# Kernel optimization log

Measured on AMD Instinct MI355X. Metric: run time of the kernel, lower is better.

## Reference

```python
import jax, jax.numpy as jnp
import numpy as np
from jax import lax

NUM_CLASSES = 10
NUM_ITERS = 3


def conv2d(x, w, b, stride):
    # x: [B,C,H,W], w: [O,I,kh,kw]
    y = lax.conv_general_dilated(x, w, (stride, stride), 'VALID',
                                 dimension_numbers=('NCHW', 'OIHW', 'NCHW'))
    return y + b[None, :, None, None]


def squash(t, axis=-1):
    sn = jnp.sum(t * t, axis=axis, keepdims=True)
    return (sn / (1.0 + sn)) * t / jnp.sqrt(sn)


def routing(x, W, num_iters=NUM_ITERS):
    # x: [B,R,Ci], W: [C,R,Ci,Co] -> outputs [B,C,Co]
    # priors[c,b,r,o] = sum_i x[b,r,i] * W[c,r,i,o]
    priors = jnp.einsum('bri,crio->cbro', x, W)  # [C,B,R,Co]
    C, B, R, Co = priors.shape
    # torch logits are [C,B,R,1,Co] but identical along Co (zeros init,
    # delta broadcast), so a [C,B,R,1] logit is mathematically identical.
    logits = jnp.zeros((C, B, R, 1), priors.dtype)
    outputs = None
    for i in range(num_iters):
        probs = jax.nn.softmax(logits, axis=2)            # over route nodes
        s = jnp.sum(probs * priors, axis=2, keepdims=True)  # [C,B,1,Co]
        outputs = squash(s, axis=-1)
        if i != num_iters - 1:
            logits = logits + jnp.sum(priors * outputs, axis=-1, keepdims=True)
    return jnp.transpose(outputs[:, :, 0, :], (1, 0, 2))  # [B,C,Co]


def setup_inputs() -> dict:
    key = jax.random.key(0)
    ks = jax.random.split(key, 16)
    B = 32
    s = 0.05
    inp = {
        'x': jax.random.normal(ks[0], (B, 1, 61, 61), jnp.float32),
        'conv0_w': jax.random.normal(ks[1], (256, 1, 9, 9), jnp.float32) * s,
        'conv0_b': jnp.zeros((256,), jnp.float32),
        'conv1_w': jax.random.normal(ks[2], (256, 256, 9, 9), jnp.float32) * s,
        'conv1_b': jnp.zeros((256,), jnp.float32),
        # 8 primary-capsule convs stacked: [8*32, 256, 9, 9]
        'prim_w': jax.random.normal(ks[3], (8 * 32, 256, 9, 9), jnp.float32) * s,
        'prim_b': jnp.zeros((8 * 32,), jnp.float32),
        'W1': jax.random.normal(ks[4], (64, 32 * 6 * 6, 8, 16), jnp.float32) * s,
        'W2': jax.random.normal(ks[5], (NUM_CLASSES, 64, 16, 16), jnp.float32) * s,
        'dec_w1': jax.random.normal(ks[6], (16 * NUM_CLASSES, 1024), jnp.float32) * s,
        'dec_b1': jnp.zeros((1024,), jnp.float32),
        'dec_w2': jax.random.normal(ks[7], (1024, 2048), jnp.float32) * s,
        'dec_b2': jnp.zeros((2048,), jnp.float32),
        'dec_w3': jax.random.normal(ks[8], (2048, 4096), jnp.float32) * s,
        'dec_b3': jnp.zeros((4096,), jnp.float32),
    }
    return inp


def reference(x, conv0_w, conv0_b, conv1_w, conv1_b, prim_w, prim_b,
              W1, W2, dec_w1, dec_b1, dec_w2, dec_b2, dec_w3, dec_b3):
    B = x.shape[0]
    h = jax.nn.relu(conv2d(x, conv0_w, conv0_b, 2))       # [B,256,27,27]
    h = jax.nn.relu(conv2d(h, conv1_w, conv1_b, 1))       # [B,256,19,19]
    # primary capsules: 8 convs of 32 channels each, k9 s2 -> [B,256,6,6]
    p = conv2d(h, prim_w, prim_b, 2)
    # torch: each capsule conv -> view(B, 32*6*6, 1), cat on last -> [B,1152,8]
    p = p.reshape(B, 8, 32 * 6 * 6)                        # [B,8,1152]
    p = jnp.transpose(p, (0, 2, 1))                        # [B,1152,8]
    p = squash(p, axis=-1)
    u = routing(p, W1)                                     # [B,64,16]
    v = routing(u, W2)                                     # [B,10,16]
    classes = jnp.sqrt(jnp.sum(v * v, axis=-1))            # [B,10]
    classes = jax.nn.softmax(classes, axis=-1)
    y = jax.nn.one_hot(jnp.argmax(classes, axis=1), NUM_CLASSES,
                       dtype=v.dtype)                       # [B,10]
    y = lax.stop_gradient(y)
    z = (v * y[:, :, None]).reshape(B, -1)                 # [B,160]
    d = jax.nn.relu(z @ dec_w1 + dec_b1)
    d = jax.nn.relu(d @ dec_w2 + dec_b2)
    reconstructions = jax.nn.sigmoid(d @ dec_w3 + dec_b3)  # [B,4096]
    return classes, reconstructions
```

## Files before the change

### kernel.cpp

```cpp
#include <hip/hip_runtime.h>
#include <hip/hip_bf16.h>
#include <math.h>


#define NB 32

typedef _Float16 f16;
typedef f16 f16x2 __attribute__((ext_vector_type(2)));
typedef f16 f16x4 __attribute__((ext_vector_type(4)));
typedef f16 f16x8 __attribute__((ext_vector_type(8)));
typedef float f32x4 __attribute__((ext_vector_type(4)));

__device__ __forceinline__ int swz(int row, int q) {
  return row * 64 + ((q * 16) ^ (((row >> 1) & 3) << 4));
}

__global__ __launch_bounds__(256) void wprep_kernel(
    const float* __restrict__ w1, const float* __restrict__ w2,
    f16* __restrict__ wo1, f16* __restrict__ wo2) {
  __shared__ f16 tile[256][82];
  int bi = blockIdx.x;
  const float* src;
  f16* dst;
  if (bi < 256) {
    src = w1 + (size_t)bi * 20736;
    dst = wo1 + bi * 256;
  } else {
    src = w2 + (size_t)(bi - 256) * 20736;
    dst = wo2 + (bi - 256) * 256;
  }
  int t = threadIdx.x;
  for (int j = t; j < 20736; j += 256) {
    int r = j / 81, c = j - r * 81;
    tile[r][c] = (f16)src[j];
  }
  __syncthreads();
  f16* d = dst + t;
  for (int tap = 0; tap < 81; ++tap)
    d[(size_t)tap * 65536] = tile[t][tap];
}

__global__ __launch_bounds__(256) void conv0_kernel(
    const float* __restrict__ x, const float* __restrict__ w,
    const float* __restrict__ bias, f16* __restrict__ outf) {
  int b = blockIdx.x, ocg = blockIdx.y, z = blockIdx.z;
  __shared__ float img[61 * 61];
  __shared__ __align__(16) float wl[81][32];
  int t = threadIdx.x;
  for (int i = t; i < 61 * 61; i += 256) img[i] = x[b * 3721 + i];
  for (int i = t; i < 81 * 32; i += 256) {
    int k = i >> 5, oc = i & 31;
    wl[k][oc] = w[(ocg * 32 + oc) * 81 + k];
  }
  __syncthreads();
  int ocs = (t & 7) * 4;
  int pg  = t >> 3;
  int oc0 = ocg * 32 + ocs;
  float b0 = bias[oc0 + 0], b1 = bias[oc0 + 1], b2 = bias[oc0 + 2],
        b3 = bias[oc0 + 3];
  for (int p = pg + z * 32; p < 729; p += 64) {
    int oh = p / 27, ow = p - oh * 27;
    float a0 = 0.f, a1 = 0.f, a2 = 0.f, a3 = 0.f;
    const float* ib = &img[oh * 2 * 61 + ow * 2];
#pragma unroll
    for (int kh = 0; kh < 9; ++kh) {
#pragma unroll
      for (int kw = 0; kw < 9; ++kw) {
        float v = ib[kh * 61 + kw];
        const float4 wv =
            *reinterpret_cast<const float4*>(&wl[kh * 9 + kw][ocs]);
        a0 += v * wv.x; a1 += v * wv.y; a2 += v * wv.z; a3 += v * wv.w;
      }
    }
    int po = oh * 28 + ow;
    f16x4 hv;
    hv[0] = (f16)fmaxf(a0 + b0, 0.f);
    hv[1] = (f16)fmaxf(a1 + b1, 0.f);
    hv[2] = (f16)fmaxf(a2 + b2, 0.f);
    hv[3] = (f16)fmaxf(a3 + b3, 0.f);
    *(f16x4*)&outf[((size_t)b * 756 + po) * 256 + oc0] = hv;
  }
}

__global__ __launch_bounds__(256, 3) void conv1_mfma(
    const f16* __restrict__ xin,
    const f16* __restrict__ wA,
    f16* __restrict__ part) {
  int b = blockIdx.x, ocg = blockIdx.y;
  int ksp = blockIdx.z >> 1, ph = blockIdx.z & 1;
  __shared__ __align__(16) f16 blds[504 * 32];
  __shared__ __align__(16) f16 alds[2][64 * 32];
  int t = threadIdx.x;
  int w = t >> 6, lane = t & 63, kg = lane >> 4, ln = lane & 15;
  int aoc = t >> 2, aq = t & 3;
  int row0 = ph * 252;
  int prow[3];
#pragma unroll
  for (int nf = 0; nf < 3; ++nf) {
    int n = ph * 192 + w * 48 + nf * 16 + ln;
    int oh = n / 20, ow = n - oh * 20;
    if (oh > 18) oh = 18;
    if (ow > 18) ow = 18;
    prow[nf] = oh * 28 + ow - row0;
  }
  f32x4 acc[4][3];
#pragma unroll
  for (int m = 0; m < 4; ++m)
#pragma unroll
    for (int nf = 0; nf < 3; ++nf) acc[m][nf] = (f32x4){0.f, 0.f, 0.f, 0.f};

  const f16* xb = xin + (size_t)b * 756 * 256 + ksp * 64;
  const f16* ab = wA + (size_t)(ocg * 64 + aoc) * 256 + ksp * 64 + aq * 8;
  for (int icc = 0; icc < 2; ++icc) {
    __syncthreads();
    for (int i = t; i < 2016; i += 256) {
      int p = i >> 2, q = i & 3;
      f16x8 v =
          *(const f16x8*)(xb + (size_t)(row0 + p) * 256 + icc * 32 + q * 8);
      *(f16x8*)((char*)blds + swz(p, q)) = v;
    }
    {
      f16x8 v = *(const f16x8*)(ab + icc * 32);
      *(f16x8*)((char*)alds[0] + swz(aoc, aq)) = v;
    }
    __syncthreads();
    for (int tap = 0; tap < 81; ++tap) {
      int cur = tap & 1;
      if (tap < 80) {
        f16x8 v = *(const f16x8*)(ab + (size_t)(tap + 1) * 65536 + icc * 32);
        *(f16x8*)((char*)alds[cur ^ 1] + swz(aoc, aq)) = v;
      }
      int kh = tap / 9, kw = tap - kh * 9;
      int shift = kh * 28 + kw;
      f16x8 af[4];
#pragma unroll
      for (int m = 0; m < 4; ++m)
        af[m] = *(const f16x8*)((const char*)alds[cur] + swz(m * 16 + ln, kg));
      f16x8 bf[3];
#pragma unroll
      for (int nf = 0; nf < 3; ++nf)
        bf[nf] =
            *(const f16x8*)((const char*)blds + swz(prow[nf] + shift, kg));
#pragma unroll
      for (int m = 0; m < 4; ++m)
#pragma unroll
        for (int nf = 0; nf < 3; ++nf)
          acc[m][nf] = __builtin_amdgcn_mfma_f32_16x16x32_f16(
              af[m], bf[nf], acc[m][nf], 0, 0, 0);
      __syncthreads();
    }
  }
  f16* pout = part + ((size_t)ksp * 32 + b) * 384 * 256 + ocg * 64;
#pragma unroll
  for (int m = 0; m < 4; ++m)
#pragma unroll
    for (int nf = 0; nf < 3; ++nf) {
      int n = ph * 192 + w * 48 + nf * 16 + ln;
      int oc = m * 16 + kg * 4;
      f16x4 v;
#pragma unroll
      for (int j = 0; j < 4; ++j) v[j] = (f16)acc[m][nf][j];
      *(f16x4*)(pout + (size_t)n * 256 + oc) = v;
    }
}

__global__ void comb1_kernel(const f16* __restrict__ part,
                             const float* __restrict__ bias,
                             f16* __restrict__ h1f) {
  int idx = blockIdx.x * 256 + threadIdx.x;
  if (idx >= 32 * 380 * 32) return;
  int ocq = idx & 31, rem = idx >> 5;
  int p = rem % 380, b = rem / 380;
  float a[8];
#pragma unroll
  for (int j = 0; j < 8; ++j) a[j] = bias[ocq * 8 + j];
#pragma unroll
  for (int k = 0; k < 4; ++k) {
    f16x8 v = *(const f16x8*)&part[(((size_t)k * 32 + b) * 384 + p) * 256 +
                                   ocq * 8];
#pragma unroll
    for (int j = 0; j < 8; ++j) a[j] += (float)v[j];
  }
  f16x8 o;
#pragma unroll
  for (int j = 0; j < 8; ++j) o[j] = (f16)fmaxf(a[j], 0.f);
  *(f16x8*)&h1f[((size_t)b * 380 + p) * 256 + ocq * 8] = o;
}

__global__ __launch_bounds__(256, 3) void prim_mfma(
    const f16* __restrict__ xin,
    const f16* __restrict__ wB,
    float* __restrict__ part2) {
  int b = blockIdx.x, ocg = blockIdx.y, ksp = blockIdx.z;
  __shared__ __align__(16) f16 blds[384 * 32];
  __shared__ __align__(16) f16 alds[2][128 * 32];
  int t = threadIdx.x;
  int w = t >> 6, lane = t & 63, kg = lane >> 4, ln = lane & 15;
  int rbase[3];
#pragma unroll
  for (int nf = 0; nf < 3; ++nf) {
    int rem = nf * 16 + ln;
    int oh6 = rem >> 3, ow6 = rem & 7;
    rbase[nf] = oh6 * 40 + ow6 * 2;
  }
  f32x4 acc[2][3];
#pragma unroll
  for (int m = 0; m < 2; ++m)
#pragma unroll
    for (int nf = 0; nf < 3; ++nf) acc[m][nf] = (f32x4){0.f, 0.f, 0.f, 0.f};

  for (int i = t; i < 1536; i += 256) {
    int pos = i >> 2, q = i & 3;
    int p = pos < 380 ? pos : pos - 20;
    f16x8 v = *(const f16x8*)(xin + ((size_t)b * 380 + p) * 256 + ksp * 32 +
                              q * 8);
    *(f16x8*)((char*)blds + swz(pos, q)) = v;
  }
  const f16* ab = wB + (size_t)(ocg * 128) * 256 + ksp * 32;
  for (int i = t; i < 512; i += 256) {
    int oc = i >> 2, q = i & 3;
    f16x8 v = *(const f16x8*)(ab + (size_t)oc * 256 + q * 8);
    *(f16x8*)((char*)alds[0] + swz(oc, q)) = v;
  }
  __syncthreads();
  for (int tap = 0; tap < 81; ++tap) {
    int cur = tap & 1;
    if (tap < 80) {
      for (int i = t; i < 512; i += 256) {
        int oc = i >> 2, q = i & 3;
        f16x8 v = *(const f16x8*)(ab + (size_t)(tap + 1) * 65536 +
                                  (size_t)oc * 256 + q * 8);
        *(f16x8*)((char*)alds[cur ^ 1] + swz(oc, q)) = v;
      }
    }
    int kh = tap / 9, kw = tap - kh * 9;
    int shift = kh * 20 + kw;
    f16x8 af[2];
#pragma unroll
    for (int m = 0; m < 2; ++m)
      af[m] = *(const f16x8*)((const char*)alds[cur] +
                              swz((w * 2 + m) * 16 + ln, kg));
    f16x8 bf[3];
#pragma unroll
    for (int nf = 0; nf < 3; ++nf)
      bf[nf] = *(const f16x8*)((const char*)blds + swz(rbase[nf] + shift, kg));
#pragma unroll
    for (int m = 0; m < 2; ++m)
#pragma unroll
      for (int nf = 0; nf < 3; ++nf)
        acc[m][nf] = __builtin_amdgcn_mfma_f32_16x16x32_f16(
            af[m], bf[nf], acc[m][nf], 0, 0, 0);
    __syncthreads();
  }
  float* pout = part2 + ((size_t)ksp * 32 + b) * 48 * 256 + ocg * 128;
#pragma unroll
  for (int m = 0; m < 2; ++m)
#pragma unroll
    for (int nf = 0; nf < 3; ++nf) {
      int n = nf * 16 + ln;
      int oc = (w * 2 + m) * 16 + kg * 4;
      *(f32x4*)(pout + (size_t)n * 256 + oc) = acc[m][nf];
    }
}

__global__ __launch_bounds__(256) void combsq_kernel(
    const float* __restrict__ part2,
    const float* __restrict__ bias, float* __restrict__ caps) {
  int bn = blockIdx.x;
  int b = bn / 48, n = bn - b * 48;
  int ow6 = n & 7;
  if (ow6 >= 6) return;
  int oh6 = n >> 3, s = oh6 * 6 + ow6;
  __shared__ float al[256];
  int oc = threadIdx.x;
  float a = 0.f;
#pragma unroll
  for (int k = 0; k < 8; ++k)
    a += part2[(((size_t)k * 32 + b) * 48 + n) * 256 + oc];
  al[oc] = a;
  __syncthreads();
  if (oc < 32) {
    int m = oc;
    float tv[8];
    float sn = 0.f;
#pragma unroll
    for (int g = 0; g < 8; ++g) {
      float v = al[g * 32 + m] + bias[g * 32 + m];
      tv[g] = v;
      sn += v * v;
    }
    float sc = sqrtf(sn) / (1.f + sn);
#pragma unroll
    for (int g = 0; g < 8; ++g)
      caps[((size_t)b * 1152 + m * 36 + s) * 8 + g] = tv[g] * sc;
  }
}

__global__ __launch_bounds__(256) void priors1_kernel(
    const float* __restrict__ x,
    const float* __restrict__ W,
    f16* __restrict__ pri) {
  int c = blockIdx.x, rt = blockIdx.y;
  int r0 = rt * 32;
  __shared__ __align__(16) float xl[32 * 32 * 8];
  int t = threadIdx.x;
  for (int q = t; q < 2048; q += 256) {
    int b = q >> 6, j = q & 63;
    *(float4*)&xl[b * 256 + j * 4] =
        *(const float4*)&x[(size_t)b * 9216 + r0 * 8 + j * 4];
  }
  int rl = t >> 3, oq = t & 7;
  float w0[8], w1[8];
#pragma unroll
  for (int i = 0; i < 8; ++i) {
    const float2 wv = *(const float2*)&W[
        (((size_t)c * 1152 + r0 + rl) * 8 + i) * 16 + 2 * oq];
    w0[i] = wv.x; w1[i] = wv.y;
  }
  __syncthreads();
  f16* pout = pri + (size_t)c * 32 * 18432 + (r0 + rl) * 16 + 2 * oq;
#pragma unroll 4
  for (int b = 0; b < 32; ++b) {
    const float4 x0 = *(const float4*)&xl[b * 256 + rl * 8];
    const float4 x1 = *(const float4*)&xl[b * 256 + rl * 8 + 4];
    float s0 = x0.x * w0[0] + x0.y * w0[1] + x0.z * w0[2] + x0.w * w0[3] +
               x1.x * w0[4] + x1.y * w0[5] + x1.z * w0[6] + x1.w * w0[7];
    float s1 = x0.x * w1[0] + x0.y * w1[1] + x0.z * w1[2] + x0.w * w1[3] +
               x1.x * w1[4] + x1.y * w1[5] + x1.z * w1[6] + x1.w * w1[7];
    f16x2 hv; hv[0] = (f16)s0; hv[1] = (f16)s1;
    *(f16x2*)(pout + (size_t)b * 18432) = hv;
  }
}

__global__ __launch_bounds__(512) void route1_kernel(
    const f16* __restrict__ pri,
    float* __restrict__ out) {
  constexpr int R = 1152;
  constexpr int NREG = 36;
  int c = blockIdx.x, b = blockIdx.y;
  __shared__ float lg[R], pr[R];
  __shared__ float redA[8], redB[8];
  __shared__ float sred[8][16];
  __shared__ float vsh[17];
  int t    = threadIdx.x;
  int o    = t & 15;
  int rhi  = t >> 4;
  int wid  = t >> 6;
  int lane = t & 63;
  const f16* pb = pri + ((size_t)c * 32 + b) * (R * 16);

  float prireg[NREG];
#pragma unroll
  for (int k = 0; k < NREG; ++k)
    prireg[k] = (float)pb[(k * 32 + rhi) * 16 + o];
  for (int r = t; r < R; r += 512) lg[r] = 0.f;
  __syncthreads();

  for (int it = 0; it < 3; ++it) {
    float lm = -1e30f;
    for (int r = t; r < R; r += 512) lm = fmaxf(lm, lg[r]);
#pragma unroll
    for (int s2 = 1; s2 <= 32; s2 <<= 1) lm = fmaxf(lm, __shfl_xor(lm, s2));
    if (lane == 0) redA[wid] = lm;
    __syncthreads();
    if (t == 0) {
      float m8 = redA[0];
#pragma unroll
      for (int w = 1; w < 8; ++w) m8 = fmaxf(m8, redA[w]);
      redA[0] = m8;
    }
    __syncthreads();
    float m = redA[0];
    float ls = 0.f;
    for (int r = t; r < R; r += 512) {
      float e = __expf(lg[r] - m);
      pr[r] = e;
      ls += e;
    }
#pragma unroll
    for (int s2 = 1; s2 <= 32; s2 <<= 1) ls += __shfl_xor(ls, s2);
    if (lane == 0) redB[wid] = ls;
    __syncthreads();
    if (t == 0) {
      float s8 = 0.f;
#pragma unroll
      for (int w = 0; w < 8; ++w) s8 += redB[w];
      redB[0] = s8;
    }
    __syncthreads();
    float denom = redB[0];
    float part = 0.f;
#pragma unroll
    for (int k = 0; k < NREG; ++k) part += pr[k * 32 + rhi] * prireg[k];
    part += __shfl_xor(part, 16);
    part += __shfl_xor(part, 32);
    if (lane < 16) sred[wid][lane] = part;
    __syncthreads();
    if (t < 16) {
      float sv = 0.f;
#pragma unroll
      for (int w = 0; w < 8; ++w) sv += sred[w][t];
      vsh[t] = sv / denom;
    }
    __syncthreads();
    if (t == 0) {
      float sn = 0.f;
#pragma unroll
      for (int oo = 0; oo < 16; ++oo) sn += vsh[oo] * vsh[oo];
      vsh[16] = sqrtf(sn) / (1.f + sn);
    }
    __syncthreads();
    if (it < 2) {
      float vo = vsh[o] * vsh[16];
#pragma unroll
      for (int k = 0; k < NREG; ++k) {
        float val = prireg[k] * vo;
        val += __shfl_xor(val, 1);
        val += __shfl_xor(val, 2);
        val += __shfl_xor(val, 4);
        val += __shfl_xor(val, 8);
        if (o == 0) lg[k * 32 + rhi] += val;
      }
      __syncthreads();
    }
  }
  if (t < 16) out[((size_t)b * 64 + c) * 16 + t] = vsh[t] * vsh[16];
}

template <int R, int CI>
__global__ __launch_bounds__(512) void routing_kernel(
    const float* __restrict__ x,
    const float* __restrict__ W,
    float* __restrict__ out) {
  constexpr int NREG = R * 16 / 512;
  int c = blockIdx.x, b = blockIdx.y;
  int C = gridDim.x;
  __shared__ float xls[R * CI];
  extern __shared__ float rdyn[];
  float* lg = rdyn;
  float* pr = rdyn + R;
  __shared__ float redA[8], redB[8];
  __shared__ float sred[8][16];
  __shared__ float vsh[17];
  int t    = threadIdx.x;
  int o    = t & 15;
  int rhi  = t >> 4;
  int wid  = t >> 6;
  int lane = t & 63;
  const float* xb = x + (size_t)b * R * CI;
  const float* Wc = W + (size_t)c * R * CI * 16;

  for (int i = t; i < R * CI; i += 512) xls[i] = xb[i];
  for (int r = t; r < R; r += 512) lg[r] = 0.f;
  __syncthreads();

  float pri[NREG];
#pragma unroll
  for (int k = 0; k < NREG; ++k) {
    int r = k * 32 + rhi;
    float s = 0.f;
#pragma unroll
    for (int i = 0; i < CI; ++i)
      s += xls[r * CI + i] * Wc[((size_t)r * CI + i) * 16 + o];
    pri[k] = s;
  }

  for (int it = 0; it < 3; ++it) {
    float lm = -1e30f;
    for (int r = t; r < R; r += 512) lm = fmaxf(lm, lg[r]);
#pragma unroll
    for (int s2 = 1; s2 <= 32; s2 <<= 1) lm = fmaxf(lm, __shfl_xor(lm, s2));
    if (lane == 0) redA[wid] = lm;
    __syncthreads();
    if (t == 0) {
      float m8 = redA[0];
#pragma unroll
      for (int w = 1; w < 8; ++w) m8 = fmaxf(m8, redA[w]);
      redA[0] = m8;
    }
    __syncthreads();
    float m = redA[0];
    float ls = 0.f;
    for (int r = t; r < R; r += 512) {
      float e = __expf(lg[r] - m);
      pr[r] = e;
      ls += e;
    }
#pragma unroll
    for (int s2 = 1; s2 <= 32; s2 <<= 1) ls += __shfl_xor(ls, s2);
    if (lane == 0) redB[wid] = ls;
    __syncthreads();
    if (t == 0) {
      float s8 = 0.f;
#pragma unroll
      for (int w = 0; w < 8; ++w) s8 += redB[w];
      redB[0] = s8;
    }
    __syncthreads();
    float denom = redB[0];
    float part = 0.f;
#pragma unroll
    for (int k = 0; k < NREG; ++k) part += pr[k * 32 + rhi] * pri[k];
    part += __shfl_xor(part, 16);
    part += __shfl_xor(part, 32);
    if (lane < 16) sred[wid][lane] = part;
    __syncthreads();
    if (t < 16) {
      float sv = 0.f;
#pragma unroll
      for (int w = 0; w < 8; ++w) sv += sred[w][t];
      vsh[t] = sv / denom;
    }
    __syncthreads();
    if (t == 0) {
      float sn = 0.f;
#pragma unroll
      for (int oo = 0; oo < 16; ++oo) sn += vsh[oo] * vsh[oo];
      vsh[16] = sqrtf(sn) / (1.f + sn);
    }
    __syncthreads();
    if (it < 2) {
      float vo = vsh[o] * vsh[16];
#pragma unroll
      for (int k = 0; k < NREG; ++k) {
        float val = pri[k] * vo;
        val += __shfl_xor(val, 1);
        val += __shfl_xor(val, 2);
        val += __shfl_xor(val, 4);
        val += __shfl_xor(val, 8);
        if (o == 0) lg[k * 32 + rhi] += val;
      }
      __syncthreads();
    }
  }
  if (t < 16) out[((size_t)b * C + c) * 16 + t] = vsh[t] * vsh[16];
}

__global__ void classes_kernel(const float* __restrict__ v,
                               float* __restrict__ outc,
                               int* __restrict__ amaxb) {
  int b = blockIdx.x;
  int t = threadIdx.x;
  __shared__ float nrm[10];
  if (t < 10) {
    float sn = 0.f;
#pragma unroll
    for (int o = 0; o < 16; ++o) {
      float xv = v[(b * 10 + t) * 16 + o];
      sn += xv * xv;
    }
    nrm[t] = sqrtf(sn);
  }
  __syncthreads();
  if (t == 0) {
    float m = nrm[0];
    int am = 0;
    for (int c = 1; c < 10; ++c)
      if (nrm[c] > m) { m = nrm[c]; am = c; }
    float s = 0.f;
    float e[10];
    for (int c = 0; c < 10; ++c) { e[c] = __expf(nrm[c] - m); s += e[c]; }
    for (int c = 0; c < 10; ++c) outc[b * 10 + c] = e[c] / s;
    amaxb[b] = am;
  }
}

__global__ __launch_bounds__(256) void fc1s_kernel(
    const float* __restrict__ v, const int* __restrict__ amaxb,
    const float* __restrict__ w, const float* __restrict__ bias,
    float* __restrict__ out) {
  int n  = blockIdx.x * 256 + threadIdx.x;
  int b0 = blockIdx.y * 8;
  __shared__ float vls[8][16];
  __shared__ int ams[8];
  int t = threadIdx.x;
  if (t < 8) ams[t] = amaxb[b0 + t];
  __syncthreads();
  if (t < 128) {
    int bb = t >> 4, oo = t & 15;
    vls[bb][oo] = v[((b0 + bb) * 10 + ams[bb]) * 16 + oo];
  }
  __syncthreads();
  float bv = bias[n];
#pragma unroll
  for (int bb = 0; bb < 8; ++bb) {
    int row0 = ams[bb] * 16;
    float acc = bv;
#pragma unroll
    for (int oo = 0; oo < 16; ++oo)
      acc += vls[bb][oo] * w[(size_t)(row0 + oo) * 1024 + n];
    out[(size_t)(b0 + bb) * 1024 + n] = fmaxf(acc, 0.f);
  }
}

template <int K, int KCH>
__global__ __launch_bounds__(256) void fcsplit_kernel(
    const float* __restrict__ in, const float* __restrict__ w,
    float* __restrict__ pbuf, int N) {
  int n  = blockIdx.x * 256 + threadIdx.x;
  int b0 = blockIdx.y * 8;
  int k0 = blockIdx.z * KCH;
  __shared__ __align__(16) float inl[KCH * 8];
  for (int idx = threadIdx.x; idx < 8 * KCH; idx += 256) {
    int bb = idx / KCH, k = idx - bb * KCH;
    inl[k * 8 + bb] = in[(size_t)(b0 + bb) * K + k0 + k];
  }
  __syncthreads();
  float acc[8];
#pragma unroll
  for (int bb = 0; bb < 8; ++bb) acc[bb] = 0.f;
  for (int k = 0; k < KCH; ++k) {
    float wv = w[(size_t)(k0 + k) * N + n];
    const float4 i0 = *reinterpret_cast<const float4*>(&inl[k * 8]);
    const float4 i1 = *reinterpret_cast<const float4*>(&inl[k * 8 + 4]);
    acc[0] += i0.x * wv; acc[1] += i0.y * wv;
    acc[2] += i0.z * wv; acc[3] += i0.w * wv;
    acc[4] += i1.x * wv; acc[5] += i1.y * wv;
    acc[6] += i1.z * wv; acc[7] += i1.w * wv;
  }
#pragma unroll
  for (int bb = 0; bb < 8; ++bb)
    pbuf[((size_t)blockIdx.z * 32 + b0 + bb) * N + n] = acc[bb];
}

template <int KS, bool RELU, bool SIG>
__global__ void fccomb_kernel(const float* __restrict__ pbuf,
                              const float* __restrict__ bias,
                              float* __restrict__ out, int N) {
  int idx = blockIdx.x * 256 + threadIdx.x;
  if (idx >= 32 * N) return;
  int b = idx / N, n = idx - b * N;
  float a = bias[n];
#pragma unroll
  for (int kz = 0; kz < KS; ++kz) a += pbuf[((size_t)kz * 32 + b) * N + n];
  if (RELU) a = fmaxf(a, 0.f);
  if (SIG)  a = 1.f / (1.f + __expf(-a));
  out[idx] = a;
}

extern "C" void kernel_launch(void* const* d_in, const int* in_sizes, int n_in,
                              void* d_out, int out_size, void* d_ws,
                              size_t ws_size, hipStream_t stream) {
  const float* x       = (const float*)d_in[0];
  const float* conv0_w = (const float*)d_in[1];
  const float* conv0_b = (const float*)d_in[2];
  const float* conv1_w = (const float*)d_in[3];
  const float* conv1_b = (const float*)d_in[4];
  const float* prim_w  = (const float*)d_in[5];
  const float* prim_b  = (const float*)d_in[6];
  const float* W1      = (const float*)d_in[7];
  const float* W2      = (const float*)d_in[8];
  const float* dec_w1  = (const float*)d_in[9];
  const float* dec_b1  = (const float*)d_in[10];
  const float* dec_w2  = (const float*)d_in[11];
  const float* dec_b2  = (const float*)d_in[12];
  const float* dec_w3  = (const float*)d_in[13];
  const float* dec_b3  = (const float*)d_in[14];
  float* out = (float*)d_out;

  float* ws    = (float*)d_ws;
  float* caps  = ws;
  float* u     = caps + 294912;
  float* vc    = u + 32768;
  int*   amaxb = (int*)(vc + 5120);
  float* trans = vc + 5120 + 32;

  f16* wA    = (f16*)trans;
  f16* wB    = wA + 5308416;
  f16* h0f   = wB + 5308416;
  f16* h1f   = h0f + 6193152;
  f16* part1 = h1f + 3112960;
  float* part2 = (float*)part1;
  f16* pri1  = (f16*)trans;
  float* d1  = trans;
  float* d2  = d1 + 32768;
  float* pb2 = d2 + 65536;
  float* pb3 = pb2 + 262144;

  wprep_kernel<<<512, 256, 0, stream>>>(conv1_w, prim_w, wA, wB);

  conv0_kernel<<<dim3(NB, 8, 2), 256, 0, stream>>>(x, conv0_w, conv0_b, h0f);

  conv1_mfma<<<dim3(NB, 4, 8), 256, 0, stream>>>(h0f, wA, part1);
  comb1_kernel<<<1520, 256, 0, stream>>>(part1, conv1_b, h1f);

  prim_mfma<<<dim3(NB, 2, 8), 256, 0, stream>>>(h1f, wB, part2);
  combsq_kernel<<<NB * 48, 256, 0, stream>>>(part2, prim_b, caps);

  priors1_kernel<<<dim3(64, 36), 256, 0, stream>>>(caps, W1, pri1);
  route1_kernel<<<dim3(64, NB), 512, 0, stream>>>(pri1, u);

  routing_kernel<64, 16>
      <<<dim3(10, NB), 512, 2 * 64 * sizeof(float), stream>>>(u, W2, vc);

  classes_kernel<<<NB, 64, 0, stream>>>(vc, out, amaxb);

  fc1s_kernel<<<dim3(4, 4), 256, 0, stream>>>(vc, amaxb, dec_w1, dec_b1, d1);

  fcsplit_kernel<1024, 256>
      <<<dim3(8, 4, 4), 256, 0, stream>>>(d1, dec_w2, pb2, 2048);
  fccomb_kernel<4, true, false>
      <<<256, 256, 0, stream>>>(pb2, dec_b2, d2, 2048);

  fcsplit_kernel<2048, 256>
      <<<dim3(16, 4, 8), 256, 0, stream>>>(d2, dec_w3, pb3, 4096);
  fccomb_kernel<8, false, true>
      <<<512, 256, 0, stream>>>(pb3, dec_b3, out + 320, 4096);
}
```

Before: 445.2 us.

## Switch conv1 to 32x32x16 MFMA and drop the output-row phase split

conv1 now uses 32x32x16 MFMA tiles instead of 16x16x32. Each block covers all 384 output positions of an image rather than half, so the grid shrinks from 1024 to 512 blocks and each activation tile is loaded into LDS once instead of being half-reloaded per phase. Each MFMA does more work per operand fetch, which cuts LDS reads per FLOP. In exchange LDS per block grows, the occupancy target drops from 3 to 2 waves per SIMD, and fewer blocks are available to fill the GPU.

```diff
diff --git a/kernel.cpp b/kernel.cpp
--- a/kernel.cpp
+++ b/kernel.cpp
@@ -10,6 +10,7 @@
 typedef f16 f16x4 __attribute__((ext_vector_type(4)));
 typedef f16 f16x8 __attribute__((ext_vector_type(8)));
 typedef float f32x4 __attribute__((ext_vector_type(4)));
+typedef float f32x16 __attribute__((ext_vector_type(16)));
 
 __device__ __forceinline__ int swz(int row, int q) {
   return row * 64 + ((q * 16) ^ (((row >> 1) & 3) << 4));
@@ -82,41 +83,41 @@
   }
 }
 
-__global__ __launch_bounds__(256, 3) void conv1_mfma(
+__global__ __launch_bounds__(256, 2) void conv1_mfma(
     const f16* __restrict__ xin,
     const f16* __restrict__ wA,
     f16* __restrict__ part) {
-  int b = blockIdx.x, ocg = blockIdx.y;
-  int ksp = blockIdx.z >> 1, ph = blockIdx.z & 1;
-  __shared__ __align__(16) f16 blds[504 * 32];
+  int b = blockIdx.x, ocg = blockIdx.y, ksp = blockIdx.z;
+  __shared__ __align__(16) f16 blds[756 * 32];
   __shared__ __align__(16) f16 alds[2][64 * 32];
   int t = threadIdx.x;
-  int w = t >> 6, lane = t & 63, kg = lane >> 4, ln = lane & 15;
+  int w = t >> 6, lane = t & 63;
+  int l31 = lane & 31, lh = lane >> 5;
   int aoc = t >> 2, aq = t & 3;
-  int row0 = ph * 252;
   int prow[3];
 #pragma unroll
   for (int nf = 0; nf < 3; ++nf) {
-    int n = ph * 192 + w * 48 + nf * 16 + ln;
+    int n = w * 96 + nf * 32 + l31;
     int oh = n / 20, ow = n - oh * 20;
     if (oh > 18) oh = 18;
     if (ow > 18) ow = 18;
-    prow[nf] = oh * 28 + ow - row0;
-  }
-  f32x4 acc[4][3];
-#pragma unroll
-  for (int m = 0; m < 4; ++m)
-#pragma unroll
-    for (int nf = 0; nf < 3; ++nf) acc[m][nf] = (f32x4){0.f, 0.f, 0.f, 0.f};
+    prow[nf] = oh * 28 + ow;
+  }
+  f32x16 acc[2][3];
+#pragma unroll
+  for (int m = 0; m < 2; ++m)
+#pragma unroll
+    for (int nf = 0; nf < 3; ++nf)
+#pragma unroll
+      for (int j = 0; j < 16; ++j) acc[m][nf][j] = 0.f;
 
   const f16* xb = xin + (size_t)b * 756 * 256 + ksp * 64;
   const f16* ab = wA + (size_t)(ocg * 64 + aoc) * 256 + ksp * 64 + aq * 8;
   for (int icc = 0; icc < 2; ++icc) {
     __syncthreads();
-    for (int i = t; i < 2016; i += 256) {
+    for (int i = t; i < 3024; i += 256) {
       int p = i >> 2, q = i & 3;
-      f16x8 v =
-          *(const f16x8*)(xb + (size_t)(row0 + p) * 256 + icc * 32 + q * 8);
+      f16x8 v = *(const f16x8*)(xb + (size_t)p * 256 + icc * 32 + q * 8);
       *(f16x8*)((char*)blds + swz(p, q)) = v;
     }
     {
@@ -132,35 +133,43 @@
       }
       int kh = tap / 9, kw = tap - kh * 9;
       int shift = kh * 28 + kw;
-      f16x8 af[4];
-#pragma unroll
-      for (int m = 0; m < 4; ++m)
-        af[m] = *(const f16x8*)((const char*)alds[cur] + swz(m * 16 + ln, kg));
-      f16x8 bf[3];
-#pragma unroll
-      for (int nf = 0; nf < 3; ++nf)
-        bf[nf] =
-            *(const f16x8*)((const char*)blds + swz(prow[nf] + shift, kg));
-#pragma unroll
-      for (int m = 0; m < 4; ++m)
+#pragma unroll
+      for (int s = 0; s < 2; ++s) {
+        int q = s * 2 + lh;
+        f16x8 af[2];
+#pragma unroll
+        for (int m = 0; m < 2; ++m)
+          af[m] =
+              *(const f16x8*)((const char*)alds[cur] + swz(m * 32 + l31, q));
+        f16x8 bf[3];
 #pragma unroll
         for (int nf = 0; nf < 3; ++nf)
-          acc[m][nf] = __builtin_amdgcn_mfma_f32_16x16x32_f16(
-              af[m], bf[nf], acc[m][nf], 0, 0, 0);
+          bf[nf] =
+              *(const f16x8*)((const char*)blds + swz(prow[nf] + shift, q));
+#pragma unroll
+        for (int m = 0; m < 2; ++m)
+#pragma unroll
+          for (int nf = 0; nf < 3; ++nf)
+            acc[m][nf] = __builtin_amdgcn_mfma_f32_32x32x16_f16(
+                af[m], bf[nf], acc[m][nf], 0, 0, 0);
+      }
       __syncthreads();
     }
   }
   f16* pout = part + ((size_t)ksp * 32 + b) * 384 * 256 + ocg * 64;
 #pragma unroll
-  for (int m = 0; m < 4; ++m)
+  for (int m = 0; m < 2; ++m)
 #pragma unroll
     for (int nf = 0; nf < 3; ++nf) {
-      int n = ph * 192 + w * 48 + nf * 16 + ln;
-      int oc = m * 16 + kg * 4;
-      f16x4 v;
-#pragma unroll
-      for (int j = 0; j < 4; ++j) v[j] = (f16)acc[m][nf][j];
-      *(f16x4*)(pout + (size_t)n * 256 + oc) = v;
+      int n = w * 96 + nf * 32 + l31;
+#pragma unroll
+      for (int g = 0; g < 4; ++g) {
+        int oc = m * 32 + 8 * g + 4 * lh;
+        f16x4 v;
+#pragma unroll
+        for (int j = 0; j < 4; ++j) v[j] = (f16)acc[m][nf][4 * g + j];
+        *(f16x4*)(pout + (size_t)n * 256 + oc) = v;
+      }
     }
 }
 
@@ -681,7 +690,7 @@
 
   conv0_kernel<<<dim3(NB, 8, 2), 256, 0, stream>>>(x, conv0_w, conv0_b, h0f);
 
-  conv1_mfma<<<dim3(NB, 4, 8), 256, 0, stream>>>(h0f, wA, part1);
+  conv1_mfma<<<dim3(NB, 4, 4), 256, 0, stream>>>(h0f, wA, part1);
   comb1_kernel<<<1520, 256, 0, stream>>>(part1, conv1_b, h1f);
 
   prim_mfma<<<dim3(NB, 2, 8), 256, 0, stream>>>(h1f, wB, part2);
```

Measured after the change: 452.4 us. No clear change (+1.6%).

## Transpose routing priors layout to o-major for vectorized f16x8 loads

Applied to the files above, without the earlier changes.

Changes the priors buffer layout from [c,b,r,o] to [c,b,o,r]. Each priors thread now handles 8 consecutive routes for one output dim, keeps 64 weights in registers, and writes f16x8 vectors. The routing kernel reads its priors with 16-byte vector loads instead of scalar f16 gathers. The priors grid shrinks from 36 to 9 route tiles per class, and each block now syncs per batch element, so the kernel gets fewer blocks and more registers per thread.

```diff
diff --git a/kernel.cpp b/kernel.cpp
--- a/kernel.cpp
+++ b/kernel.cpp
@@ -301,34 +301,35 @@
     const float* __restrict__ W,
     f16* __restrict__ pri) {
   int c = blockIdx.x, rt = blockIdx.y;
-  int r0 = rt * 32;
-  __shared__ __align__(16) float xl[32 * 32 * 8];
+  int r0 = rt * 128;
+  __shared__ __align__(16) float xl[128 * 8];
   int t = threadIdx.x;
-  for (int q = t; q < 2048; q += 256) {
-    int b = q >> 6, j = q & 63;
-    *(float4*)&xl[b * 256 + j * 4] =
-        *(const float4*)&x[(size_t)b * 9216 + r0 * 8 + j * 4];
-  }
-  int rl = t >> 3, oq = t & 7;
-  float w0[8], w1[8];
-#pragma unroll
-  for (int i = 0; i < 8; ++i) {
-    const float2 wv = *(const float2*)&W[
-        (((size_t)c * 1152 + r0 + rl) * 8 + i) * 16 + 2 * oq];
-    w0[i] = wv.x; w1[i] = wv.y;
-  }
-  __syncthreads();
-  f16* pout = pri + (size_t)c * 32 * 18432 + (r0 + rl) * 16 + 2 * oq;
-#pragma unroll 4
+  int o = t & 15, rb = t >> 4;
+  float wreg[8][8];
+#pragma unroll
+  for (int j = 0; j < 8; ++j) {
+    int r = r0 + rb * 8 + j;
+#pragma unroll
+    for (int i = 0; i < 8; ++i)
+      wreg[j][i] = W[(((size_t)c * 1152 + r) * 8 + i) * 16 + o];
+  }
+  f16* pout = pri + (((size_t)c * 32) * 16 + o) * 1152 + r0 + rb * 8;
   for (int b = 0; b < 32; ++b) {
-    const float4 x0 = *(const float4*)&xl[b * 256 + rl * 8];
-    const float4 x1 = *(const float4*)&xl[b * 256 + rl * 8 + 4];
-    float s0 = x0.x * w0[0] + x0.y * w0[1] + x0.z * w0[2] + x0.w * w0[3] +
-               x1.x * w0[4] + x1.y * w0[5] + x1.z * w0[6] + x1.w * w0[7];
-    float s1 = x0.x * w1[0] + x0.y * w1[1] + x0.z * w1[2] + x0.w * w1[3] +
-               x1.x * w1[4] + x1.y * w1[5] + x1.z * w1[6] + x1.w * w1[7];
-    f16x2 hv; hv[0] = (f16)s0; hv[1] = (f16)s1;
-    *(f16x2*)(pout + (size_t)b * 18432) = hv;
+    __syncthreads();
+    *(float4*)&xl[t * 4] =
+        *(const float4*)&x[(size_t)b * 9216 + r0 * 8 + t * 4];
+    __syncthreads();
+    f16x8 hv;
+#pragma unroll
+    for (int j = 0; j < 8; ++j) {
+      const float4 x0 = *(const float4*)&xl[(rb * 8 + j) * 8];
+      const float4 x1 = *(const float4*)&xl[(rb * 8 + j) * 8 + 4];
+      float s = x0.x * wreg[j][0] + x0.y * wreg[j][1] + x0.z * wreg[j][2] +
+                x0.w * wreg[j][3] + x1.x * wreg[j][4] + x1.y * wreg[j][5] +
+                x1.z * wreg[j][6] + x1.w * wreg[j][7];
+      hv[j] = (f16)s;
+    }
+    *(f16x8*)(pout + (size_t)b * (16 * 1152)) = hv;
   }
 }
 
@@ -336,7 +337,6 @@
     const f16* __restrict__ pri,
     float* __restrict__ out) {
   constexpr int R = 1152;
-  constexpr int NREG = 36;
   int c = blockIdx.x, b = blockIdx.y;
   __shared__ float lg[R], pr[R];
   __shared__ float redA[8], redB[8];
@@ -344,15 +344,16 @@
   __shared__ float vsh[17];
   int t    = threadIdx.x;
   int o    = t & 15;
-  int rhi  = t >> 4;
+  int rg   = t >> 4;
   int wid  = t >> 6;
   int lane = t & 63;
-  const f16* pb = pri + ((size_t)c * 32 + b) * (R * 16);
-
-  float prireg[NREG];
-#pragma unroll
-  for (int k = 0; k < NREG; ++k)
-    prireg[k] = (float)pb[(k * 32 + rhi) * 16 + o];
+  const f16* pb = pri + (((size_t)c * 32 + b) * 16 + o) * R;
+  bool has5 = (rg < 16);
+  f16x8 prih[5];
+#pragma unroll
+  for (int k = 0; k < 4; ++k)
+    prih[k] = *(const f16x8*)(pb + k * 256 + rg * 8);
+  prih[4] = has5 ? *(const f16x8*)(pb + 1024 + rg * 8) : (f16x8)(f16)0.f;
   for (int r = t; r < R; r += 512) lg[r] = 0.f;
   __syncthreads();
 
@@ -391,7 +392,16 @@
     float denom = redB[0];
     float part = 0.f;
 #pragma unroll
-    for (int k = 0; k < NREG; ++k) part += pr[k * 32 + rhi] * prireg[k];
+    for (int k = 0; k < 4; ++k) {
+      const float* pp = &pr[k * 256 + rg * 8];
+#pragma unroll
+      for (int j = 0; j < 8; ++j) part += pp[j] * (float)prih[k][j];
+    }
+    if (has5) {
+      const float* pp = &pr[1024 + rg * 8];
+#pragma unroll
+      for (int j = 0; j < 8; ++j) part += pp[j] * (float)prih[4][j];
+    }
     part += __shfl_xor(part, 16);
     part += __shfl_xor(part, 32);
     if (lane < 16) sred[wid][lane] = part;
@@ -413,13 +423,27 @@
     if (it < 2) {
       float vo = vsh[o] * vsh[16];
 #pragma unroll
-      for (int k = 0; k < NREG; ++k) {
-        float val = prireg[k] * vo;
-        val += __shfl_xor(val, 1);
-        val += __shfl_xor(val, 2);
-        val += __shfl_xor(val, 4);
-        val += __shfl_xor(val, 8);
-        if (o == 0) lg[k * 32 + rhi] += val;
+      for (int k = 0; k < 4; ++k) {
+#pragma unroll
+        for (int j = 0; j < 8; ++j) {
+          float val = (float)prih[k][j] * vo;
+          val += __shfl_xor(val, 1);
+          val += __shfl_xor(val, 2);
+          val += __shfl_xor(val, 4);
+          val += __shfl_xor(val, 8);
+          if (o == 0) lg[k * 256 + rg * 8 + j] += val;
+        }
+      }
+      if (has5) {
+#pragma unroll
+        for (int j = 0; j < 8; ++j) {
+          float val = (float)prih[4][j] * vo;
+          val += __shfl_xor(val, 1);
+          val += __shfl_xor(val, 2);
+          val += __shfl_xor(val, 4);
+          val += __shfl_xor(val, 8);
+          if (o == 0) lg[1024 + rg * 8 + j] += val;
+        }
       }
       __syncthreads();
     }
@@ -687,7 +711,7 @@
   prim_mfma<<<dim3(NB, 2, 8), 256, 0, stream>>>(h1f, wB, part2);
   combsq_kernel<<<NB * 48, 256, 0, stream>>>(part2, prim_b, caps);
 
-  priors1_kernel<<<dim3(64, 36), 256, 0, stream>>>(caps, W1, pri1);
+  priors1_kernel<<<dim3(64, 9), 256, 0, stream>>>(caps, W1, pri1);
   route1_kernel<<<dim3(64, NB), 512, 0, stream>>>(pri1, u);
 
   routing_kernel<64, 16>
```

Measured after the change: 451.8 us. Within noise of the previous version (+1.5%).
